# Kernel tuning notes

Hardware: AMD Instinct MI355X
Metric: run time of the kernel (lower is better)

## Reference

```python
import jax, jax.numpy as jnp
import numpy as np

B, S, D = 4, 2048, 1024


def setup_inputs() -> dict:
    key = jax.random.key(0)
    ks = jax.random.split(key, 7)
    scale = 1.0 / np.sqrt(D)  # mimic torch Linear default init scale
    x = jax.random.normal(ks[0], (B, S, D), dtype=jnp.float32)
    Wq = jax.random.uniform(ks[1], (D, D), jnp.float32, -scale, scale)
    bq = jax.random.uniform(ks[2], (D,), jnp.float32, -scale, scale)
    Wk = jax.random.uniform(ks[3], (D, D), jnp.float32, -scale, scale)
    bk = jax.random.uniform(ks[4], (D,), jnp.float32, -scale, scale)
    Wv = jax.random.uniform(ks[5], (D, D), jnp.float32, -scale, scale)
    bv = jax.random.uniform(ks[6], (D,), jnp.float32, -scale, scale)
    return {"x": x, "Wq": Wq, "bq": bq, "Wk": Wk, "bk": bk, "Wv": Wv, "bv": bv}


def reference(x, Wq, bq, Wk, bk, Wv, bv):
    # Linear projections (torch Linear: x @ W.T + b; here W stored as [in, out])
    q = jnp.einsum("bsd,de->bse", x, Wq) + bq
    k = jnp.einsum("bsd,de->bse", x, Wk) + bk
    v = jnp.einsum("bsd,de->bse", x, Wv) + bv
    # NOTE: original module applies NO 1/sqrt(d) scaling — faithful to source.
    scores = jnp.einsum("bqd,bkd->bqk", q, k)  # [B, S, S]
    attn = jax.nn.softmax(scores, axis=-1)
    return jnp.einsum("bqk,bkd->bqd", attn, v)
```

## Files before the change

### kernel.cpp

```cpp
#include <hip/hip_runtime.h>
#include <stdint.h>

typedef unsigned short ushort_t;
typedef _Float16 f16;
typedef __attribute__((ext_vector_type(8))) _Float16 half8;
typedef __attribute__((ext_vector_type(4))) _Float16 half4;
typedef __attribute__((ext_vector_type(4))) float float4v;

#define AS1 __attribute__((address_space(1)))
#define AS3 __attribute__((address_space(3)))

static __device__ __forceinline__ void gload16(const void* g, void* l) {
    __builtin_amdgcn_global_load_lds((const AS1 unsigned int*)g,
                                     (AS3 unsigned int*)l, 16, 0, 0);
}

template<int OUT, bool BIAS>
__global__ __launch_bounds__(256)
void gemm_k(const f16* __restrict__ A, const f16* __restrict__ B,
            const float* __restrict__ bias,
            float* __restrict__ Cf, f16* __restrict__ Ch, f16* __restrict__ Vt,
            int K, int lda, int ldb, int ldc,
            long zsA, long zsB, long zsC)
{
    extern __shared__ f16 smem[];
    f16* sA = smem;
    f16* sB = smem + 4096;

    const long zb = blockIdx.z;
    A += zb * zsA; B += zb * zsB;

    const int t  = threadIdx.x;
    const int bm = blockIdx.x * 128;
    const int bn = blockIdx.y * 128;

    const int  srow = t >> 2;
    const int  skg  = (t & 3) * 8;
    const f16* gA = A + (long)(bm + srow) * lda + skg;
    const f16* gB = B + (long)(bn + srow) * ldb + skg;
    const long rstepA = (long)64 * lda;
    const long rstepB = (long)64 * ldb;

    const int lane = t & 63;
    const int wv   = t >> 6;
    const int wm   = (wv & 1) * 64;
    const int wn   = (wv >> 1) * 64;
    const int lm   = lane & 15;
    const int q    = lane >> 4;

    float4v acc[4][4];
    #pragma unroll
    for (int i = 0; i < 4; ++i)
        #pragma unroll
        for (int j = 0; j < 4; ++j)
            #pragma unroll
            for (int r = 0; r < 4; ++r) acc[i][j][r] = 0.f;

    for (int kt = 0; kt < K; kt += 32) {
        __syncthreads();
        #pragma unroll
        for (int r = 0; r < 2; ++r) {
            gload16(gA + kt + r * rstepA, sA + r * 2048 + t * 8);
            gload16(gB + kt + r * rstepB, sB + r * 2048 + t * 8);
        }
        __syncthreads();

        half8 a[4], b[4];
        #pragma unroll
        for (int i = 0; i < 4; ++i) {
            a[i] = *(const half8*)(sA + (wm + i * 16 + lm) * 32 + q * 8);
            b[i] = *(const half8*)(sB + (wn + i * 16 + lm) * 32 + q * 8);
        }
        #pragma unroll
        for (int i = 0; i < 4; ++i)
            #pragma unroll
            for (int j = 0; j < 4; ++j)
                acc[i][j] = __builtin_amdgcn_mfma_f32_16x16x32_f16(a[i], b[j], acc[i][j], 0, 0, 0);
    }

    #pragma unroll
    for (int i = 0; i < 4; ++i) {
        const int rowb = bm + wm + i * 16 + q * 4;
        #pragma unroll
        for (int j = 0; j < 4; ++j) {
            const int col = bn + wn + j * 16 + lm;
            const float bv_ = BIAS ? bias[col] : 0.f;
            if (OUT == 4 && col >= 2048) {
                half4 pk;
                #pragma unroll
                for (int r = 0; r < 4; ++r) pk[r] = (f16)(acc[i][j][r] + bv_);
                *(half4*)(Vt + ((long)(rowb >> 11) * 1024 + (col - 2048)) * 2048 + (rowb & 2047)) = pk;
            } else {
                #pragma unroll
                for (int r = 0; r < 4; ++r) {
                    const float val = acc[i][j][r] + bv_;
                    const int row = rowb + r;
                    if (OUT == 0) Cf[zb * zsC + (long)row * ldc + col] = val;
                    else          Ch[(long)row * ldc + col] = (f16)val;
                }
            }
        }
    }
}

__global__ __launch_bounds__(256)
void convert_x_k(const float* __restrict__ X, f16* __restrict__ H)
{
    const long i = ((long)blockIdx.x * 256 + threadIdx.x) * 4;
    const float4v v = *(const float4v*)(X + i);
    half4 h;
    #pragma unroll
    for (int j = 0; j < 4; ++j) h[j] = (f16)v[j];
    *(half4*)(H + i) = h;
}

__global__ __launch_bounds__(256)
void transpose_w_k(const float* __restrict__ Wq, const float* __restrict__ Wk,
                   const float* __restrict__ Wv, f16* __restrict__ WT)
{
    __shared__ float tile[64][65];
    const int z = blockIdx.z;
    const float* W = (z == 0) ? Wq : (z == 1) ? Wk : Wv;
    f16* T = WT + (long)z * 1048576;

    const int t  = threadIdx.x;
    const int n0 = blockIdx.x * 64;
    const int k0 = blockIdx.y * 64;
    #pragma unroll
    for (int i = 0; i < 4; ++i) {
        const int r = (t >> 4) + i * 16;
        const int c = (t & 15) * 4;
        const float4v v = *(const float4v*)(W + (long)(k0 + r) * 1024 + n0 + c);
        tile[r][c + 0] = v[0]; tile[r][c + 1] = v[1];
        tile[r][c + 2] = v[2]; tile[r][c + 3] = v[3];
    }
    __syncthreads();
    #pragma unroll
    for (int i = 0; i < 4; ++i) {
        const int nr = (t >> 4) + i * 16;
        const int c  = (t & 15) * 4;
        half4 h;
        #pragma unroll
        for (int j = 0; j < 4; ++j) h[j] = (f16)tile[c + j][nr];
        *(half4*)(T + (long)(n0 + nr) * 1024 + k0 + c) = h;
    }
}

__global__ __launch_bounds__(256)
void bias_concat_k(const float* __restrict__ bq, const float* __restrict__ bk,
                   const float* __restrict__ bv, float* __restrict__ bqkv)
{
    const int i = blockIdx.x * 256 + threadIdx.x;
    bqkv[i] = (i < 1024) ? bq[i] : (i < 2048) ? bk[i - 1024] : bv[i - 2048];
}

__global__ __launch_bounds__(256)
void softmax_k(const float* __restrict__ Sc, f16* __restrict__ P)
{
    const int t = threadIdx.x;
    const long row = blockIdx.x;
    const float4v* src = (const float4v*)(Sc + row * 2048);
    float4v x0 = src[t];
    float4v x1 = src[t + 256];

    float m = -1e30f;
    #pragma unroll
    for (int j = 0; j < 4; ++j) { m = fmaxf(m, x0[j]); m = fmaxf(m, x1[j]); }
    #pragma unroll
    for (int off = 32; off; off >>= 1) m = fmaxf(m, __shfl_xor(m, off, 64));
    __shared__ float r1[4], r2[4];
    if ((t & 63) == 0) r1[t >> 6] = m;
    __syncthreads();
    m = fmaxf(fmaxf(r1[0], r1[1]), fmaxf(r1[2], r1[3]));

    float s = 0.f;
    float4v e0, e1;
    #pragma unroll
    for (int j = 0; j < 4; ++j) {
        e0[j] = __expf(x0[j] - m); s += e0[j];
        e1[j] = __expf(x1[j] - m); s += e1[j];
    }
    #pragma unroll
    for (int off = 32; off; off >>= 1) s += __shfl_xor(s, off, 64);
    if ((t & 63) == 0) r2[t >> 6] = s;
    __syncthreads();
    s = r2[0] + r2[1] + r2[2] + r2[3];
    const float inv = 1.f / s;

    half4 p0, p1;
    #pragma unroll
    for (int j = 0; j < 4; ++j) { p0[j] = (f16)(e0[j] * inv); p1[j] = (f16)(e1[j] * inv); }
    half4* dst = (half4*)(P + row * 2048);
    dst[t] = p0;
    dst[t + 256] = p1;
}

extern "C" void kernel_launch(void* const* d_in, const int* in_sizes, int n_in,
                              void* d_out, int out_size, void* d_ws, size_t ws_size,
                              hipStream_t stream)
{
    const float* x  = (const float*)d_in[0];
    const float* Wq = (const float*)d_in[1];
    const float* bq = (const float*)d_in[2];
    const float* Wk = (const float*)d_in[3];
    const float* bk = (const float*)d_in[4];
    const float* Wv = (const float*)d_in[5];
    const float* bv = (const float*)d_in[6];
    float* out = (float*)d_out;

    char* ws = (char*)d_ws;
    const long MiB = 1024 * 1024;
    f16*   xh   = (f16*)  (ws + 0);
    f16*   WT   = (f16*)  (ws + 16 * MiB);
    float* bqkv = (float*)(ws + 22 * MiB);
    float* scores = (float*)(ws + 0);
    f16*   qk     = (f16*) (ws + 64 * MiB);
    f16*   vT     = (f16*) (ws + 96 * MiB);
    f16*   attn   = (f16*) (ws + 112 * MiB);

    convert_x_k<<<8192, 256, 0, stream>>>(x, xh);
    transpose_w_k<<<dim3(16, 16, 3), 256, 0, stream>>>(Wq, Wk, Wv, WT);
    bias_concat_k<<<12, 256, 0, stream>>>(bq, bk, bv, bqkv);

    gemm_k<4, true><<<dim3(64, 24, 1), 256, 16384, stream>>>(
        xh, WT, bqkv, nullptr, qk, vT,
        1024, 1024, 1024, 2048, 0, 0, 0);

    const long SS = (long)2048 * 2048;
    gemm_k<0, false><<<dim3(16, 16, 4), 256, 16384, stream>>>(
        qk, qk + 1024, nullptr, scores, nullptr, nullptr,
        1024, 2048, 2048, 2048, SS, SS, SS);
    softmax_k<<<8192, 256, 0, stream>>>(scores, attn);
    gemm_k<0, false><<<dim3(16, 8, 4), 256, 16384, stream>>>(
        attn, vT, nullptr, out, nullptr, nullptr,
        2048, 2048, 2048, 1024, SS, (long)1024 * 2048, (long)2048 * 1024);
}
```

Baseline: 309.8 us.

## Load GEMM B operand directly to registers, store scores as fp16, fuse preprocessing

The GEMM now stages only A through LDS, with a K step of 64 split into two halves. B fragments are loaded straight from global memory into registers and prefetched one step ahead. The score matrix is written as fp16 instead of fp32, and softmax normalises it in place, which cuts score traffic and drops the separate attention buffer. The three preprocessing kernels are merged into one launch. The risks are fp16 rounding or overflow of the unscaled scores, since they are not divided by sqrt(d) and may be large, and uncoalesced direct global loads for B.

```diff
diff --git a/kernel.cpp b/kernel.cpp
--- a/kernel.cpp
+++ b/kernel.cpp
@@ -24,8 +24,8 @@
             long zsA, long zsB, long zsC)
 {
     extern __shared__ f16 smem[];
-    f16* sA = smem;
-    f16* sB = smem + 4096;
+    f16* sA0 = smem;
+    f16* sA1 = smem + 4096;
 
     const long zb = blockIdx.z;
     A += zb * zsA; B += zb * zsB;
@@ -37,9 +37,7 @@
     const int  srow = t >> 2;
     const int  skg  = (t & 3) * 8;
     const f16* gA = A + (long)(bm + srow) * lda + skg;
-    const f16* gB = B + (long)(bn + srow) * ldb + skg;
     const long rstepA = (long)64 * lda;
-    const long rstepB = (long)64 * ldb;
 
     const int lane = t & 63;
     const int wv   = t >> 6;
@@ -48,6 +46,9 @@
     const int lm   = lane & 15;
     const int q    = lane >> 4;
 
+    const f16* Bb = B + (long)(bn + wn + lm) * ldb + q * 8;
+    const long jstep = (long)16 * ldb;
+
     float4v acc[4][4];
     #pragma unroll
     for (int i = 0; i < 4; ++i)
@@ -56,26 +57,43 @@
             #pragma unroll
             for (int r = 0; r < 4; ++r) acc[i][j][r] = 0.f;
 
-    for (int kt = 0; kt < K; kt += 32) {
+    half8 b0[4], b1[4];
+    #pragma unroll
+    for (int j = 0; j < 4; ++j) b0[j] = *(const half8*)(Bb + j * jstep);
+
+    for (int kt = 0; kt < K; kt += 64) {
         __syncthreads();
         #pragma unroll
         for (int r = 0; r < 2; ++r) {
-            gload16(gA + kt + r * rstepA, sA + r * 2048 + t * 8);
-            gload16(gB + kt + r * rstepB, sB + r * 2048 + t * 8);
-        }
+            gload16(gA + kt      + r * rstepA, sA0 + r * 2048 + t * 8);
+            gload16(gA + kt + 32 + r * rstepA, sA1 + r * 2048 + t * 8);
+        }
+        #pragma unroll
+        for (int j = 0; j < 4; ++j) b1[j] = *(const half8*)(Bb + j * jstep + kt + 32);
         __syncthreads();
 
-        half8 a[4], b[4];
-        #pragma unroll
-        for (int i = 0; i < 4; ++i) {
-            a[i] = *(const half8*)(sA + (wm + i * 16 + lm) * 32 + q * 8);
-            b[i] = *(const half8*)(sB + (wn + i * 16 + lm) * 32 + q * 8);
-        }
+        half8 a[4];
+        #pragma unroll
+        for (int i = 0; i < 4; ++i)
+            a[i] = *(const half8*)(sA0 + (wm + i * 16 + lm) * 32 + q * 8);
         #pragma unroll
         for (int i = 0; i < 4; ++i)
             #pragma unroll
             for (int j = 0; j < 4; ++j)
-                acc[i][j] = __builtin_amdgcn_mfma_f32_16x16x32_f16(a[i], b[j], acc[i][j], 0, 0, 0);
+                acc[i][j] = __builtin_amdgcn_mfma_f32_16x16x32_f16(a[i], b0[j], acc[i][j], 0, 0, 0);
+
+        const int ktn = (kt + 64 < K) ? kt + 64 : 0;
+        #pragma unroll
+        for (int j = 0; j < 4; ++j) b0[j] = *(const half8*)(Bb + j * jstep + ktn);
+
+        #pragma unroll
+        for (int i = 0; i < 4; ++i)
+            a[i] = *(const half8*)(sA1 + (wm + i * 16 + lm) * 32 + q * 8);
+        #pragma unroll
+        for (int i = 0; i < 4; ++i)
+            #pragma unroll
+            for (int j = 0; j < 4; ++j)
+                acc[i][j] = __builtin_amdgcn_mfma_f32_16x16x32_f16(a[i], b1[j], acc[i][j], 0, 0, 0);
     }
 
     #pragma unroll
@@ -95,8 +113,9 @@
                 for (int r = 0; r < 4; ++r) {
                     const float val = acc[i][j][r] + bv_;
                     const int row = rowb + r;
-                    if (OUT == 0) Cf[zb * zsC + (long)row * ldc + col] = val;
-                    else          Ch[(long)row * ldc + col] = (f16)val;
+                    if (OUT == 0)      Cf[zb * zsC + (long)row * ldc + col] = val;
+                    else if (OUT == 1) Ch[zb * zsC + (long)row * ldc + col] = (f16)val;
+                    else               Ch[(long)row * ldc + col] = (f16)val;
                 }
             }
         }
@@ -104,68 +123,70 @@
 }
 
 __global__ __launch_bounds__(256)
-void convert_x_k(const float* __restrict__ X, f16* __restrict__ H)
-{
-    const long i = ((long)blockIdx.x * 256 + threadIdx.x) * 4;
-    const float4v v = *(const float4v*)(X + i);
-    half4 h;
-    #pragma unroll
-    for (int j = 0; j < 4; ++j) h[j] = (f16)v[j];
-    *(half4*)(H + i) = h;
+void preproc_k(const float* __restrict__ x,
+               const float* __restrict__ Wq, const float* __restrict__ Wk,
+               const float* __restrict__ Wv,
+               const float* __restrict__ bq, const float* __restrict__ bk,
+               const float* __restrict__ bv,
+               f16* __restrict__ xh, f16* __restrict__ WT, float* __restrict__ bqkv)
+{
+    __shared__ float tile[64][65];
+    const int bx = blockIdx.x;
+    const int t  = threadIdx.x;
+
+    if (bx < 8192) {
+        const long i = ((long)bx * 256 + t) * 4;
+        const float4v v = *(const float4v*)(x + i);
+        half4 h;
+        #pragma unroll
+        for (int j = 0; j < 4; ++j) h[j] = (f16)v[j];
+        *(half4*)(xh + i) = h;
+    } else if (bx < 8960) {
+        const int f = bx - 8192;
+        const int z = f >> 8;
+        const int rem = f & 255;
+        const int n0 = (rem & 15) * 64;
+        const int k0 = (rem >> 4) * 64;
+        const float* W = (z == 0) ? Wq : (z == 1) ? Wk : Wv;
+        f16* T = WT + (long)z * 1048576;
+        #pragma unroll
+        for (int i = 0; i < 4; ++i) {
+            const int r = (t >> 4) + i * 16;
+            const int c = (t & 15) * 4;
+            const float4v v = *(const float4v*)(W + (long)(k0 + r) * 1024 + n0 + c);
+            tile[r][c + 0] = v[0]; tile[r][c + 1] = v[1];
+            tile[r][c + 2] = v[2]; tile[r][c + 3] = v[3];
+        }
+        __syncthreads();
+        #pragma unroll
+        for (int i = 0; i < 4; ++i) {
+            const int nr = (t >> 4) + i * 16;
+            const int c  = (t & 15) * 4;
+            half4 h;
+            #pragma unroll
+            for (int j = 0; j < 4; ++j) h[j] = (f16)tile[c + j][nr];
+            *(half4*)(T + (long)(n0 + nr) * 1024 + k0 + c) = h;
+        }
+    } else {
+        const int i = (bx - 8960) * 256 + t;
+        bqkv[i] = (i < 1024) ? bq[i] : (i < 2048) ? bk[i - 1024] : bv[i - 2048];
+    }
 }
 
 __global__ __launch_bounds__(256)
-void transpose_w_k(const float* __restrict__ Wq, const float* __restrict__ Wk,
-                   const float* __restrict__ Wv, f16* __restrict__ WT)
-{
-    __shared__ float tile[64][65];
-    const int z = blockIdx.z;
-    const float* W = (z == 0) ? Wq : (z == 1) ? Wk : Wv;
-    f16* T = WT + (long)z * 1048576;
-
-    const int t  = threadIdx.x;
-    const int n0 = blockIdx.x * 64;
-    const int k0 = blockIdx.y * 64;
-    #pragma unroll
-    for (int i = 0; i < 4; ++i) {
-        const int r = (t >> 4) + i * 16;
-        const int c = (t & 15) * 4;
-        const float4v v = *(const float4v*)(W + (long)(k0 + r) * 1024 + n0 + c);
-        tile[r][c + 0] = v[0]; tile[r][c + 1] = v[1];
-        tile[r][c + 2] = v[2]; tile[r][c + 3] = v[3];
-    }
-    __syncthreads();
-    #pragma unroll
-    for (int i = 0; i < 4; ++i) {
-        const int nr = (t >> 4) + i * 16;
-        const int c  = (t & 15) * 4;
-        half4 h;
-        #pragma unroll
-        for (int j = 0; j < 4; ++j) h[j] = (f16)tile[c + j][nr];
-        *(half4*)(T + (long)(n0 + nr) * 1024 + k0 + c) = h;
-    }
-}
-
-__global__ __launch_bounds__(256)
-void bias_concat_k(const float* __restrict__ bq, const float* __restrict__ bk,
-                   const float* __restrict__ bv, float* __restrict__ bqkv)
-{
-    const int i = blockIdx.x * 256 + threadIdx.x;
-    bqkv[i] = (i < 1024) ? bq[i] : (i < 2048) ? bk[i - 1024] : bv[i - 2048];
-}
-
-__global__ __launch_bounds__(256)
-void softmax_k(const float* __restrict__ Sc, f16* __restrict__ P)
+void softmax_k(f16* __restrict__ Sc)
 {
     const int t = threadIdx.x;
     const long row = blockIdx.x;
-    const float4v* src = (const float4v*)(Sc + row * 2048);
-    float4v x0 = src[t];
-    float4v x1 = src[t + 256];
+    half8* p = (half8*)(Sc + row * 2048);
+    const half8 hv = p[t];
+    float xv[8];
+    #pragma unroll
+    for (int j = 0; j < 8; ++j) xv[j] = (float)hv[j];
 
     float m = -1e30f;
     #pragma unroll
-    for (int j = 0; j < 4; ++j) { m = fmaxf(m, x0[j]); m = fmaxf(m, x1[j]); }
+    for (int j = 0; j < 8; ++j) m = fmaxf(m, xv[j]);
     #pragma unroll
     for (int off = 32; off; off >>= 1) m = fmaxf(m, __shfl_xor(m, off, 64));
     __shared__ float r1[4], r2[4];
@@ -174,12 +195,8 @@
     m = fmaxf(fmaxf(r1[0], r1[1]), fmaxf(r1[2], r1[3]));
 
     float s = 0.f;
-    float4v e0, e1;
-    #pragma unroll
-    for (int j = 0; j < 4; ++j) {
-        e0[j] = __expf(x0[j] - m); s += e0[j];
-        e1[j] = __expf(x1[j] - m); s += e1[j];
-    }
+    #pragma unroll
+    for (int j = 0; j < 8; ++j) { xv[j] = __expf(xv[j] - m); s += xv[j]; }
     #pragma unroll
     for (int off = 32; off; off >>= 1) s += __shfl_xor(s, off, 64);
     if ((t & 63) == 0) r2[t >> 6] = s;
@@ -187,12 +204,10 @@
     s = r2[0] + r2[1] + r2[2] + r2[3];
     const float inv = 1.f / s;
 
-    half4 p0, p1;
-    #pragma unroll
-    for (int j = 0; j < 4; ++j) { p0[j] = (f16)(e0[j] * inv); p1[j] = (f16)(e1[j] * inv); }
-    half4* dst = (half4*)(P + row * 2048);
-    dst[t] = p0;
-    dst[t + 256] = p1;
+    half8 o;
+    #pragma unroll
+    for (int j = 0; j < 8; ++j) o[j] = (f16)(xv[j] * inv);
+    p[t] = o;
 }
 
 extern "C" void kernel_launch(void* const* d_in, const int* in_sizes, int n_in,
@@ -213,25 +228,22 @@
     f16*   xh   = (f16*)  (ws + 0);
     f16*   WT   = (f16*)  (ws + 16 * MiB);
     float* bqkv = (float*)(ws + 22 * MiB);
-    float* scores = (float*)(ws + 0);
+    f16*   scores = (f16*) (ws + 0);
     f16*   qk     = (f16*) (ws + 64 * MiB);
     f16*   vT     = (f16*) (ws + 96 * MiB);
-    f16*   attn   = (f16*) (ws + 112 * MiB);
-
-    convert_x_k<<<8192, 256, 0, stream>>>(x, xh);
-    transpose_w_k<<<dim3(16, 16, 3), 256, 0, stream>>>(Wq, Wk, Wv, WT);
-    bias_concat_k<<<12, 256, 0, stream>>>(bq, bk, bv, bqkv);
+
+    preproc_k<<<8972, 256, 0, stream>>>(x, Wq, Wk, Wv, bq, bk, bv, xh, WT, bqkv);
 
     gemm_k<4, true><<<dim3(64, 24, 1), 256, 16384, stream>>>(
         xh, WT, bqkv, nullptr, qk, vT,
         1024, 1024, 1024, 2048, 0, 0, 0);
 
     const long SS = (long)2048 * 2048;
-    gemm_k<0, false><<<dim3(16, 16, 4), 256, 16384, stream>>>(
-        qk, qk + 1024, nullptr, scores, nullptr, nullptr,
+    gemm_k<1, false><<<dim3(16, 16, 4), 256, 16384, stream>>>(
+        qk, qk + 1024, nullptr, nullptr, scores, nullptr,
         1024, 2048, 2048, 2048, SS, SS, SS);
-    softmax_k<<<8192, 256, 0, stream>>>(scores, attn);
+    softmax_k<<<8192, 256, 0, stream>>>(scores);
     gemm_k<0, false><<<dim3(16, 8, 4), 256, 16384, stream>>>(
-        attn, vT, nullptr, out, nullptr, nullptr,
+        scores, vT, nullptr, out, nullptr, nullptr,
         2048, 2048, 2048, 1024, SS, (long)1024 * 2048, (long)2048 * 1024);
 }
```

After: 381.6 us. 23.2% more time.
